# Performance work log

Measured on AMD Instinct MI355X. Metric: run time of the kernel, lower is better.

Reference implementation:

```python
import jax, jax.numpy as jnp
import numpy as np

B_, T_, D_, H_ = 16, 512, 256, 256
SCALE = 0.1


def setup_inputs() -> dict:
    key = jax.random.key(0)
    ks = jax.random.split(key, 4)
    s = 0.05  # xavier-ish init scale
    return {
        "x": jax.random.normal(ks[0], (B_, T_, D_), dtype=jnp.float32),
        "W_w": jax.random.normal(ks[1], (4 * H_, D_), dtype=jnp.float32) * s,
        "W_b": jnp.zeros((4 * H_,), dtype=jnp.float32),
        "U_w": jax.random.normal(ks[2], (4 * H_, H_), dtype=jnp.float32) * s,
        "U_b": jnp.zeros((4 * H_,), dtype=jnp.float32),
        "B_w": jax.random.normal(ks[3], (H_, D_, H_), dtype=jnp.float32) * s,
        "B_b": jnp.zeros((H_,), dtype=jnp.float32),
    }


def reference(x, W_w, W_b, U_w, U_b, B_w, B_b):
    # x: [B,T,D]; W_w: [4H,D]; U_w: [4H,H]; B_w: [H,D,H] (torch Bilinear layout)
    B, T, D = x.shape
    H = U_w.shape[1]
    # Precompute the input projection for all timesteps in one big GEMM
    Wx = jnp.einsum('btd,gd->btg', x, W_w) + W_b  # [B,T,4H]

    def step(carry, inp):
        h, c = carry
        wx_t, x_t = inp  # [B,4H], [B,D]
        gates = wx_t + h @ U_w.T + U_b
        i, f, o, g = jnp.split(gates, 4, axis=-1)
        i = jax.nn.sigmoid(i)
        f = jax.nn.sigmoid(f)
        o = jax.nn.sigmoid(o)
        g = jnp.tanh(g)
        # torch Bilinear: out[b,o] = sum_{d,h} x[b,d] W[o,d,h] h[b,h] + bias
        m = jnp.tanh(jnp.einsum('bd,odh,bh->bo', x_t, B_w, h) + B_b)
        c = f * c + i * g + SCALE * m
        h = o * jnp.tanh(c)
        return (h, c), h

    h0 = jnp.zeros((B, H), dtype=x.dtype)
    c0 = jnp.zeros((B, H), dtype=x.dtype)
    (h, c), outs = jax.lax.scan(
        step, (h0, c0), (jnp.swapaxes(Wx, 0, 1), jnp.swapaxes(x, 0, 1)))
    return jnp.swapaxes(outs, 0, 1), (h, c)  # ([B,T,H], ([B,H],[B,H]))
```

## Files before the change

### kernel.cpp

```cpp
#include <hip/hip_runtime.h>

typedef unsigned short u16;
typedef unsigned int u32;
typedef unsigned long long u64;
typedef short s16x8 __attribute__((ext_vector_type(8)));
typedef float f32x4 __attribute__((ext_vector_type(4)));
typedef __bf16 bf16x2 __attribute__((ext_vector_type(2)));

#define BTH 2097152

__device__ __forceinline__ u16 f2bf(float f) {
  u32 u = __float_as_uint(f);
  u32 r = (u + 0x7FFFu + ((u >> 16) & 1u)) >> 16;
  return (u16)r;
}
__device__ __forceinline__ float bf2f(u16 u) {
  return __uint_as_float(((u32)u) << 16);
}
__device__ __forceinline__ float sigm_(float x) { return 1.f / (1.f + __expf(-x)); }
__device__ __forceinline__ float tanh_(float x) {
  x = fminf(15.f, fmaxf(-15.f, x));
  float e = __expf(2.f * x);
  return (e - 1.f) / (e + 1.f);
}

#if defined(__has_builtin)
#if __has_builtin(__builtin_amdgcn_fdot2_f32_bf16)
#define HAVE_BF16_DOT2 1
#endif
#endif

__device__ __forceinline__ float dotp(u32 a, u32 b, float acc) {
#ifdef HAVE_BF16_DOT2
  return __builtin_amdgcn_fdot2_f32_bf16(__builtin_bit_cast(bf16x2, a),
                                         __builtin_bit_cast(bf16x2, b), acc, false);
#else
  acc += bf2f((u16)(a & 0xFFFFu)) * bf2f((u16)(b & 0xFFFFu));
  acc += bf2f((u16)(a >> 16)) * bf2f((u16)(b >> 16));
  return acc;
#endif
}

__device__ __forceinline__ void async_cp16(const u16* g, u16* l) {
  __builtin_amdgcn_global_load_lds(
      (const __attribute__((address_space(1))) void*)g,
      (__attribute__((address_space(3))) void*)l, 16, 0, 0);
}

__global__ __launch_bounds__(256) void prep_kernel(
    const float* __restrict__ x, const float* __restrict__ Ww,
    const float* __restrict__ Uw, const float* __restrict__ Bw,
    u16* __restrict__ xb, u16* __restrict__ Wbt, u16* __restrict__ Ubt,
    u16* __restrict__ Btt, u64* __restrict__ stz) {
  const int bid = blockIdx.x;
  const int tid = threadIdx.x;
  if (bid < 8192) {
    int e = bid * 256 + tid;
    int d = e & 255;
    int r = e >> 8;
    int bb = r >> 9, t = r & 511;
    xb[(size_t)((t << 4) | bb) * 256 + d] = f2bf(x[e]);
  } else if (bid < 9216) {
    int e = (bid - 8192) * 256 + tid;
    Wbt[e] = f2bf(Ww[e]);
  } else if (bid < 10240) {
    int e = (bid - 9216) * 256 + tid;
    Ubt[e] = f2bf(Uw[e]);
  } else if (bid < 14336) {
    __shared__ float T[64][65];
    int tb = bid - 10240;
    int o = tb >> 4, xi = tb & 15;
    const int d0 = (xi >> 2) * 64;
    const int h0 = (xi & 3) * 64;
    const float* src = Bw + (size_t)o * 65536;
#pragma unroll
    for (int k = 0; k < 16; ++k) {
      int idx = tid + k * 256;
      int rr = idx >> 6, cc = idx & 63;
      T[rr][cc] = src[(size_t)(d0 + rr) * 256 + h0 + cc];
    }
    __syncthreads();
#pragma unroll
    for (int k = 0; k < 16; ++k) {
      int idx = tid + k * 256;
      int rr = idx >> 6, cc = idx & 63;
      Btt[(size_t)(o * 256 + h0 + rr) * 256 + d0 + cc] = f2bf(T[cc][rr]);
    }
  } else {
    for (int i = tid; i < 6144; i += 256) stz[i] = 0ull;
  }
}

__global__ __launch_bounds__(512, 2) void fused_kernel(
    const u16* __restrict__ Ysc, const float* __restrict__ wx,
    const u16* __restrict__ Ubt, const float* __restrict__ Bb,
    float* cbuf, u64* hdata, float* __restrict__ out, int t0, int Tcur,
    const u16* __restrict__ Ag, const u16* __restrict__ Bg,
    u16* __restrict__ Ygm,
    const u16* __restrict__ Wbt, const float* __restrict__ Wb,
    const float* __restrict__ Ub, float* __restrict__ wxout,
    int sblocks, int wxblocks) {
  __shared__ __align__(16) char smem[24576];
  const int tid = threadIdx.x;
  if ((int)blockIdx.x >= sblocks) {
    u16* As = (u16*)smem;
    u16* Bs = (u16*)(smem + 8192);
    const int gi = (int)blockIdx.x - sblocks;
    const bool iswx = gi < wxblocks;
    int mt, n0;
    const u16* Bop;
    if (iswx) {
      mt = gi >> 2;
      n0 = (gi & 3) * 256;
      Bop = Wbt;
    } else {
      int g2 = gi - wxblocks;
      mt = g2 >> 8;
      n0 = (g2 & 255) * 256;
      Bop = Bg;
    }
    const u16* A = Ag + (size_t)mt * 128 * 256;
    const int wave = tid >> 6, lane = tid & 63;
    const int wm = (wave >> 2) * 64, wn = (wave & 3) * 64;
    const int qm = lane & 15, quad = lane >> 4;
    f32x4 acc[4][4] = {};
    const size_t ga = (size_t)(tid >> 2) * 256 + (tid & 3) * 8;
    const int c0 = tid, c1 = tid + 512;
    const size_t gb0 = (size_t)(n0 + (c0 >> 2)) * 256 + (c0 & 3) * 8;
    const size_t gb1 = (size_t)(n0 + (c1 >> 2)) * 256 + (c1 & 3) * 8;
    for (int k0 = 0; k0 < 256; k0 += 32) {
      __syncthreads();
      async_cp16(A + ga + k0, As + tid * 8);
      async_cp16(Bop + gb0 + k0, Bs + c0 * 8);
      async_cp16(Bop + gb1 + k0, Bs + c1 * 8);
      __syncthreads();
      s16x8 af[4], bfr[4];
#pragma unroll
      for (int i = 0; i < 4; ++i)
        af[i] = *(const s16x8*)&As[(wm + i * 16 + qm) * 32 + quad * 8];
#pragma unroll
      for (int j = 0; j < 4; ++j)
        bfr[j] = *(const s16x8*)&Bs[(wn + j * 16 + qm) * 32 + quad * 8];
#pragma unroll
      for (int i = 0; i < 4; ++i)
#pragma unroll
        for (int j = 0; j < 4; ++j)
          acc[i][j] = __builtin_amdgcn_mfma_f32_16x16x32_bf16(af[i], bfr[j], acc[i][j], 0, 0, 0);
    }
    if (iswx) {
#pragma unroll
      for (int i = 0; i < 4; ++i) {
        int rg = mt * 128 + wm + i * 16 + quad * 4;
#pragma unroll
        for (int j = 0; j < 4; ++j) {
          int cg = n0 + wn + j * 16 + qm;
          float bias = Wb[cg] + Ub[cg];
#pragma unroll
          for (int r = 0; r < 4; ++r)
            wxout[(size_t)(rg + r) * 1024 + cg] = acc[i][j][r] + bias;
        }
      }
    } else {
#pragma unroll
      for (int i = 0; i < 4; ++i) {
        int rg = wm + i * 16 + quad * 4;
#pragma unroll
        for (int j = 0; j < 4; ++j) {
          int cg = n0 + wn + j * 16 + qm;
#pragma unroll
          for (int r = 0; r < 4; ++r)
            Ygm[(size_t)(mt * 128 + rg + r) * 65536 + cg] = f2bf(acc[i][j][r]);
        }
      }
    }
    return;
  }
  u32(*lh)[128] = (u32(*)[128])smem;
  int* lflag = (int*)(smem + 1024);
  const int b = blockIdx.x >> 2;
  const int p = blockIdx.x & 3;
  const int oo = tid >> 3;
  const int s = tid & 7;
  const int o = (p << 6) + oo;
  const int wave = tid >> 6;
  const int lane = tid & 63;

  uint4 Ur[4][4];
  const uint4* Ub4 = (const uint4*)Ubt;
#pragma unroll
  for (int g = 0; g < 4; ++g) {
    int row = (g << 8) + o;
#pragma unroll
    for (int j = 0; j < 4; ++j) Ur[g][j] = Ub4[(size_t)row * 32 + s * 4 + j];
  }

  float c = cbuf[(b << 8) + o];
  const float bbias = Bb[o];
  if (tid < 2) lflag[tid] = t0 - 1;

  const int tend = t0 + Tcur;
  const u16* Yp = Ysc + (size_t)b * 65536 + (size_t)o * 256 + s * 32;
  uint4 Yc[4];
  {
    const uint4* y0 = (const uint4*)Yp;
    Yc[0] = y0[0]; Yc[1] = y0[1]; Yc[2] = y0[2]; Yc[3] = y0[3];
  }
  const float* wxp0 = wx + ((size_t)t0 * 16 + b) * 1024 + o;
  float w0 = wxp0[0], w1 = wxp0[256], w2 = wxp0[512], w3 = wxp0[768];
  float hn = 0.f;
  u64* hg = hdata + ((size_t)b << 8);
  __syncthreads();

  for (int t = t0; t < tend; ++t) {
    int dn = (t + 1 < tend) ? (t + 1 - t0) : (t - t0);
    const uint4* ynp = (const uint4*)(Yp + (size_t)dn * 1048576);
    uint4 yn0 = ynp[0], yn1 = ynp[1], yn2 = ynp[2], yn3 = ynp[3];
    int tn = (t + 1 < tend) ? (t + 1) : t;
    const float* nwp = wx + ((size_t)tn * 16 + b) * 1024 + o;
    float nw0 = nwp[0], nw1 = nwp[256], nw2 = nwp[512], nw3 = nwp[768];

    const int par = t & 1;
    if (wave == 0) {
      const u64* hp = hg + (par << 7) + (lane << 1);
      u64 v0, v1;
      for (;;) {
        v0 = __hip_atomic_load(hp, __ATOMIC_RELAXED, __HIP_MEMORY_SCOPE_AGENT);
        v1 = __hip_atomic_load(hp + 1, __ATOMIC_RELAXED, __HIP_MEMORY_SCOPE_AGENT);
        int ok = ((u32)(v0 >> 32) == (u32)t) & ((u32)(v1 >> 32) == (u32)t);
        if (__all(ok)) break;
      }
      lh[par][(lane << 1)] = (u32)v0;
      lh[par][(lane << 1) + 1] = (u32)v1;
      __hip_atomic_store(&lflag[par], t, __ATOMIC_RELEASE, __HIP_MEMORY_SCOPE_WORKGROUP);
    } else {
      while (__hip_atomic_load(&lflag[par], __ATOMIC_ACQUIRE, __HIP_MEMORY_SCOPE_WORKGROUP) < t) {}
    }

    uint4 hq[4];
    {
      const uint4* lp = (const uint4*)&lh[par][s << 4];
      hq[0] = lp[0]; hq[1] = lp[1]; hq[2] = lp[2]; hq[3] = lp[3];
    }

    float a0 = 0.f, a1 = 0.f, a2 = 0.f, a3 = 0.f, am = 0.f;
#pragma unroll
    for (int j = 0; j < 4; ++j) {
      u32 h0 = hq[j].x, h1 = hq[j].y, h2 = hq[j].z, h3 = hq[j].w;
      a0 = dotp(Ur[0][j].x, h0, a0); a0 = dotp(Ur[0][j].y, h1, a0);
      a0 = dotp(Ur[0][j].z, h2, a0); a0 = dotp(Ur[0][j].w, h3, a0);
      a1 = dotp(Ur[1][j].x, h0, a1); a1 = dotp(Ur[1][j].y, h1, a1);
      a1 = dotp(Ur[1][j].z, h2, a1); a1 = dotp(Ur[1][j].w, h3, a1);
      a2 = dotp(Ur[2][j].x, h0, a2); a2 = dotp(Ur[2][j].y, h1, a2);
      a2 = dotp(Ur[2][j].z, h2, a2); a2 = dotp(Ur[2][j].w, h3, a2);
      a3 = dotp(Ur[3][j].x, h0, a3); a3 = dotp(Ur[3][j].y, h1, a3);
      a3 = dotp(Ur[3][j].z, h2, a3); a3 = dotp(Ur[3][j].w, h3, a3);
      am = dotp(Yc[j].x, h0, am);   am = dotp(Yc[j].y, h1, am);
      am = dotp(Yc[j].z, h2, am);   am = dotp(Yc[j].w, h3, am);
    }
#pragma unroll
    for (int mk = 1; mk < 8; mk <<= 1) {
      a0 += __shfl_xor(a0, mk, 8);
      a1 += __shfl_xor(a1, mk, 8);
      a2 += __shfl_xor(a2, mk, 8);
      a3 += __shfl_xor(a3, mk, 8);
      am += __shfl_xor(am, mk, 8);
    }
    float gi = sigm_(a0 + w0);
    float gf = sigm_(a1 + w1);
    float go = sigm_(a2 + w2);
    float gg = tanh_(a3 + w3);
    float mm = tanh_(am + bbias);
    c = gf * c + gi * gg + 0.1f * mm;
    hn = go * tanh_(c);

    float hnext = __shfl_down(hn, 8);
    if (s == 0) {
      if (!(oo & 1)) {
        u32 pk = (u32)f2bf(hn) | ((u32)f2bf(hnext) << 16);
        u64 pk64 = ((u64)(u32)(t + 1) << 32) | (u64)pk;
        __hip_atomic_store(hg + (((size_t)((t + 1) & 1)) << 7) + (p << 5) + (oo >> 1),
                           pk64, __ATOMIC_RELAXED, __HIP_MEMORY_SCOPE_AGENT);
      }
      out[((size_t)b * 512 + t) * 256 + o] = hn;
    }
    Yc[0] = yn0; Yc[1] = yn1; Yc[2] = yn2; Yc[3] = yn3;
    w0 = nw0; w1 = nw1; w2 = nw2; w3 = nw3;
  }
  if (s == 0) {
    cbuf[(b << 8) + o] = c;
    out[(size_t)BTH + (b << 8) + o] = hn;
    out[(size_t)BTH + 4096 + (b << 8) + o] = c;
  }
}

extern "C" void kernel_launch(void* const* d_in, const int* in_sizes, int n_in,
                              void* d_out, int out_size, void* d_ws, size_t ws_size,
                              hipStream_t stream) {
  const float* x  = (const float*)d_in[0];
  const float* Ww = (const float*)d_in[1];
  const float* Wb = (const float*)d_in[2];
  const float* Uw = (const float*)d_in[3];
  const float* Ub = (const float*)d_in[4];
  const float* Bw = (const float*)d_in[5];
  const float* Bb = (const float*)d_in[6];
  float* out = (float*)d_out;

  char* ws = (char*)d_ws;
  const size_t WX_B  = (size_t)512 * 16 * 1024 * 4;
  const size_t XB_B  = (size_t)8192 * 256 * 2;
  const size_t BTT_B = (size_t)65536 * 256 * 2;
  const size_t WBT_B = (size_t)1024 * 256 * 2;
  const size_t UBT_B = (size_t)1024 * 256 * 2;
  const size_t CB_B  = 16384;
  const size_t HD_B  = 32768;
  const size_t ST_B  = CB_B + HD_B;
  const size_t fixedB = WX_B + XB_B + BTT_B + WBT_B + UBT_B + ST_B;
  size_t avail = (ws_size > fixedB) ? (ws_size - fixedB) : 0;
  long Tc = (long)(avail / (2 * 2097152));
  if (Tc > 64) Tc = 64;
  Tc &= ~7L;
  if (Tc < 8) Tc = 8;

  size_t YB   = (size_t)Tc * 2097152;
  u16* Y0     = (u16*)ws;
  u16* Y1     = (u16*)(ws + YB);
  float* wx   = (float*)(ws + 2 * YB);
  u16* xb     = (u16*)(ws + 2 * YB + WX_B);
  u16* Btt    = (u16*)(ws + 2 * YB + WX_B + XB_B);
  u16* Wbt    = (u16*)(ws + 2 * YB + WX_B + XB_B + BTT_B);
  u16* Ubt    = (u16*)(ws + 2 * YB + WX_B + XB_B + BTT_B + WBT_B);
  char* st    = ws + 2 * YB + WX_B + XB_B + BTT_B + WBT_B + UBT_B;
  float* cbuf = (float*)st;
  u64* hdata  = (u64*)(st + CB_B);

  prep_kernel<<<14337, 256, 0, stream>>>(x, Ww, Uw, Bw, xb, Wbt, Ubt, Btt, (u64*)st);

  {
    int Tc0 = (int)Tc;
    int ng0 = (Tc0 * 16 / 128) * 256;
    fused_kernel<<<256 + ng0, 512, 0, stream>>>(
        nullptr, wx, Ubt, Bb, cbuf, hdata, out, 0, 0,
        xb, Btt, Y0, Wbt, Wb, Ub, wx, 0, 256);
  }
  int cidx = 0;
  for (int t0 = 0; t0 < 512; t0 += (int)Tc, ++cidx) {
    int Tcur = (512 - t0 < (int)Tc) ? (512 - t0) : (int)Tc;
    int t0n = t0 + Tcur;
    u16* Ysc = (cidx & 1) ? Y1 : Y0;
    u16* Ygm = (cidx & 1) ? Y0 : Y1;
    int ng = 0;
    const u16* Ag = xb;
    if (t0n < 512) {
      int Tcn = (512 - t0n < (int)Tc) ? (512 - t0n) : (int)Tc;
      ng = (Tcn * 16 / 128) * 256;
      Ag = xb + (size_t)t0n * 4096;
    }
    fused_kernel<<<64 + ng, 512, 0, stream>>>(
        Ysc, wx, Ubt, Bb, cbuf, hdata, out, t0, Tcur,
        Ag, Btt, Ygm, Wbt, Wb, Ub, wx, 64, 0);
  }
}
```

Before: 1.356 ms.

## Process two batch rows per recurrent block to halve recurrent block count

Each recurrent workgroup now handles two independent batch sequences (b and b+8), interleaving their LSTM steps so one sequence's compute can overlap the other's wait for cross-block h exchange. This halves the recurrent blocks from 64 to 32, freeing CUs for the concurrent GEMM blocks. The Y-tile stores from the GEMM path become nontemporal. Per-thread work and register pressure double (two Y caches, two cell states), and the serial per-step latency may grow.

```diff
diff --git a/kernel.cpp b/kernel.cpp
--- a/kernel.cpp
+++ b/kernel.cpp
@@ -45,6 +45,47 @@
   __builtin_amdgcn_global_load_lds(
       (const __attribute__((address_space(1))) void*)g,
       (__attribute__((address_space(3))) void*)l, 16, 0, 0);
+}
+
+__device__ __forceinline__ void lstm_step(
+    const uint4 (&Ur)[4][4], const uint4 (&Yc)[4], const u32* hrow,
+    float w0, float w1, float w2, float w3, float bbias,
+    float& c, float& hn) {
+  uint4 hq[4];
+  {
+    const uint4* lp = (const uint4*)hrow;
+    hq[0] = lp[0]; hq[1] = lp[1]; hq[2] = lp[2]; hq[3] = lp[3];
+  }
+  float a0 = 0.f, a1 = 0.f, a2 = 0.f, a3 = 0.f, am = 0.f;
+#pragma unroll
+  for (int j = 0; j < 4; ++j) {
+    u32 h0 = hq[j].x, h1 = hq[j].y, h2 = hq[j].z, h3 = hq[j].w;
+    a0 = dotp(Ur[0][j].x, h0, a0); a0 = dotp(Ur[0][j].y, h1, a0);
+    a0 = dotp(Ur[0][j].z, h2, a0); a0 = dotp(Ur[0][j].w, h3, a0);
+    a1 = dotp(Ur[1][j].x, h0, a1); a1 = dotp(Ur[1][j].y, h1, a1);
+    a1 = dotp(Ur[1][j].z, h2, a1); a1 = dotp(Ur[1][j].w, h3, a1);
+    a2 = dotp(Ur[2][j].x, h0, a2); a2 = dotp(Ur[2][j].y, h1, a2);
+    a2 = dotp(Ur[2][j].z, h2, a2); a2 = dotp(Ur[2][j].w, h3, a2);
+    a3 = dotp(Ur[3][j].x, h0, a3); a3 = dotp(Ur[3][j].y, h1, a3);
+    a3 = dotp(Ur[3][j].z, h2, a3); a3 = dotp(Ur[3][j].w, h3, a3);
+    am = dotp(Yc[j].x, h0, am);   am = dotp(Yc[j].y, h1, am);
+    am = dotp(Yc[j].z, h2, am);   am = dotp(Yc[j].w, h3, am);
+  }
+#pragma unroll
+  for (int mk = 1; mk < 8; mk <<= 1) {
+    a0 += __shfl_xor(a0, mk, 8);
+    a1 += __shfl_xor(a1, mk, 8);
+    a2 += __shfl_xor(a2, mk, 8);
+    a3 += __shfl_xor(a3, mk, 8);
+    am += __shfl_xor(am, mk, 8);
+  }
+  float gi = sigm_(a0 + w0);
+  float gf = sigm_(a1 + w1);
+  float go = sigm_(a2 + w2);
+  float gg = tanh_(a3 + w3);
+  float mm = tanh_(am + bbias);
+  c = gf * c + gi * gg + 0.1f * mm;
+  hn = go * tanh_(c);
 }
 
 __global__ __launch_bounds__(256) void prep_kernel(
@@ -169,15 +210,17 @@
           int cg = n0 + wn + j * 16 + qm;
 #pragma unroll
           for (int r = 0; r < 4; ++r)
-            Ygm[(size_t)(mt * 128 + rg + r) * 65536 + cg] = f2bf(acc[i][j][r]);
+            __builtin_nontemporal_store(
+                f2bf(acc[i][j][r]),
+                &Ygm[(size_t)(mt * 128 + rg + r) * 65536 + cg]);
         }
       }
     }
     return;
   }
-  u32(*lh)[128] = (u32(*)[128])smem;
-  int* lflag = (int*)(smem + 1024);
-  const int b = blockIdx.x >> 2;
+  u32(*lh)[2][128] = (u32(*)[2][128])smem;
+  int* lflag = (int*)(smem + 4096);
+  const int bh = blockIdx.x >> 2;
   const int p = blockIdx.x & 3;
   const int oo = tid >> 3;
   const int s = tid & 7;
@@ -194,34 +237,34 @@
     for (int j = 0; j < 4; ++j) Ur[g][j] = Ub4[(size_t)row * 32 + s * 4 + j];
   }
 
-  float c = cbuf[(b << 8) + o];
   const float bbias = Bb[o];
-  if (tid < 2) lflag[tid] = t0 - 1;
+  float cA = cbuf[(bh << 8) + o];
+  float cB = cbuf[((bh + 8) << 8) + o];
+  if (tid < 4) lflag[tid] = t0 - 1;
 
   const int tend = t0 + Tcur;
-  const u16* Yp = Ysc + (size_t)b * 65536 + (size_t)o * 256 + s * 32;
-  uint4 Yc[4];
+  const u16* YpA = Ysc + (size_t)bh * 65536 + (size_t)o * 256 + s * 32;
+  const u16* YpB = YpA + (size_t)8 * 65536;
+  uint4 YcA[4], YcB[4];
   {
-    const uint4* y0 = (const uint4*)Yp;
-    Yc[0] = y0[0]; Yc[1] = y0[1]; Yc[2] = y0[2]; Yc[3] = y0[3];
-  }
-  const float* wxp0 = wx + ((size_t)t0 * 16 + b) * 1024 + o;
-  float w0 = wxp0[0], w1 = wxp0[256], w2 = wxp0[512], w3 = wxp0[768];
-  float hn = 0.f;
-  u64* hg = hdata + ((size_t)b << 8);
+    const uint4* ya = (const uint4*)YpA;
+    YcA[0] = ya[0]; YcA[1] = ya[1]; YcA[2] = ya[2]; YcA[3] = ya[3];
+    const uint4* yb = (const uint4*)YpB;
+    YcB[0] = yb[0]; YcB[1] = yb[1]; YcB[2] = yb[2]; YcB[3] = yb[3];
+  }
+  const float* wxpA0 = wx + ((size_t)t0 * 16 + bh) * 1024 + o;
+  float wA0 = wxpA0[0], wA1 = wxpA0[256], wA2 = wxpA0[512], wA3 = wxpA0[768];
+  const float* wxpB0 = wxpA0 + 8 * 1024;
+  float wB0 = wxpB0[0], wB1 = wxpB0[256], wB2 = wxpB0[512], wB3 = wxpB0[768];
+  float hnA = 0.f, hnB = 0.f;
+  u64* hgA = hdata + ((size_t)bh << 8);
+  u64* hgB = hdata + ((size_t)(bh + 8) << 8);
   __syncthreads();
 
   for (int t = t0; t < tend; ++t) {
-    int dn = (t + 1 < tend) ? (t + 1 - t0) : (t - t0);
-    const uint4* ynp = (const uint4*)(Yp + (size_t)dn * 1048576);
-    uint4 yn0 = ynp[0], yn1 = ynp[1], yn2 = ynp[2], yn3 = ynp[3];
-    int tn = (t + 1 < tend) ? (t + 1) : t;
-    const float* nwp = wx + ((size_t)tn * 16 + b) * 1024 + o;
-    float nw0 = nwp[0], nw1 = nwp[256], nw2 = nwp[512], nw3 = nwp[768];
-
     const int par = t & 1;
     if (wave == 0) {
-      const u64* hp = hg + (par << 7) + (lane << 1);
+      const u64* hp = hgA + (par << 7) + (lane << 1);
       u64 v0, v1;
       for (;;) {
         v0 = __hip_atomic_load(hp, __ATOMIC_RELAXED, __HIP_MEMORY_SCOPE_AGENT);
@@ -229,67 +272,74 @@
         int ok = ((u32)(v0 >> 32) == (u32)t) & ((u32)(v1 >> 32) == (u32)t);
         if (__all(ok)) break;
       }
-      lh[par][(lane << 1)] = (u32)v0;
-      lh[par][(lane << 1) + 1] = (u32)v1;
+      lh[0][par][(lane << 1)] = (u32)v0;
+      lh[0][par][(lane << 1) + 1] = (u32)v1;
       __hip_atomic_store(&lflag[par], t, __ATOMIC_RELEASE, __HIP_MEMORY_SCOPE_WORKGROUP);
-    } else {
-      while (__hip_atomic_load(&lflag[par], __ATOMIC_ACQUIRE, __HIP_MEMORY_SCOPE_WORKGROUP) < t) {}
-    }
-
-    uint4 hq[4];
+    } else if (wave == 1) {
+      const u64* hp = hgB + (par << 7) + (lane << 1);
+      u64 v0, v1;
+      for (;;) {
+        v0 = __hip_atomic_load(hp, __ATOMIC_RELAXED, __HIP_MEMORY_SCOPE_AGENT);
+        v1 = __hip_atomic_load(hp + 1, __ATOMIC_RELAXED, __HIP_MEMORY_SCOPE_AGENT);
+        int ok = ((u32)(v0 >> 32) == (u32)t) & ((u32)(v1 >> 32) == (u32)t);
+        if (__all(ok)) break;
+      }
+      lh[1][par][(lane << 1)] = (u32)v0;
+      lh[1][par][(lane << 1) + 1] = (u32)v1;
+      __hip_atomic_store(&lflag[2 + par], t, __ATOMIC_RELEASE, __HIP_MEMORY_SCOPE_WORKGROUP);
+    }
+    int dn = (t + 1 < tend) ? (t + 1 - t0) : (t - t0);
+    int tn = (t + 1 < tend) ? (t + 1) : t;
+
+    while (__hip_atomic_load(&lflag[par], __ATOMIC_ACQUIRE, __HIP_MEMORY_SCOPE_WORKGROUP) < t) {}
+    lstm_step(Ur, YcA, &lh[0][par][s << 4], wA0, wA1, wA2, wA3, bbias, cA, hnA);
     {
-      const uint4* lp = (const uint4*)&lh[par][s << 4];
-      hq[0] = lp[0]; hq[1] = lp[1]; hq[2] = lp[2]; hq[3] = lp[3];
-    }
-
-    float a0 = 0.f, a1 = 0.f, a2 = 0.f, a3 = 0.f, am = 0.f;
-#pragma unroll
-    for (int j = 0; j < 4; ++j) {
-      u32 h0 = hq[j].x, h1 = hq[j].y, h2 = hq[j].z, h3 = hq[j].w;
-      a0 = dotp(Ur[0][j].x, h0, a0); a0 = dotp(Ur[0][j].y, h1, a0);
-      a0 = dotp(Ur[0][j].z, h2, a0); a0 = dotp(Ur[0][j].w, h3, a0);
-      a1 = dotp(Ur[1][j].x, h0, a1); a1 = dotp(Ur[1][j].y, h1, a1);
-      a1 = dotp(Ur[1][j].z, h2, a1); a1 = dotp(Ur[1][j].w, h3, a1);
-      a2 = dotp(Ur[2][j].x, h0, a2); a2 = dotp(Ur[2][j].y, h1, a2);
-      a2 = dotp(Ur[2][j].z, h2, a2); a2 = dotp(Ur[2][j].w, h3, a2);
-      a3 = dotp(Ur[3][j].x, h0, a3); a3 = dotp(Ur[3][j].y, h1, a3);
-      a3 = dotp(Ur[3][j].z, h2, a3); a3 = dotp(Ur[3][j].w, h3, a3);
-      am = dotp(Yc[j].x, h0, am);   am = dotp(Yc[j].y, h1, am);
-      am = dotp(Yc[j].z, h2, am);   am = dotp(Yc[j].w, h3, am);
-    }
-#pragma unroll
-    for (int mk = 1; mk < 8; mk <<= 1) {
-      a0 += __shfl_xor(a0, mk, 8);
-      a1 += __shfl_xor(a1, mk, 8);
-      a2 += __shfl_xor(a2, mk, 8);
-      a3 += __shfl_xor(a3, mk, 8);
-      am += __shfl_xor(am, mk, 8);
-    }
-    float gi = sigm_(a0 + w0);
-    float gf = sigm_(a1 + w1);
-    float go = sigm_(a2 + w2);
-    float gg = tanh_(a3 + w3);
-    float mm = tanh_(am + bbias);
-    c = gf * c + gi * gg + 0.1f * mm;
-    hn = go * tanh_(c);
-
-    float hnext = __shfl_down(hn, 8);
-    if (s == 0) {
-      if (!(oo & 1)) {
-        u32 pk = (u32)f2bf(hn) | ((u32)f2bf(hnext) << 16);
-        u64 pk64 = ((u64)(u32)(t + 1) << 32) | (u64)pk;
-        __hip_atomic_store(hg + (((size_t)((t + 1) & 1)) << 7) + (p << 5) + (oo >> 1),
-                           pk64, __ATOMIC_RELAXED, __HIP_MEMORY_SCOPE_AGENT);
-      }
-      out[((size_t)b * 512 + t) * 256 + o] = hn;
-    }
-    Yc[0] = yn0; Yc[1] = yn1; Yc[2] = yn2; Yc[3] = yn3;
-    w0 = nw0; w1 = nw1; w2 = nw2; w3 = nw3;
+      float hnext = __shfl_down(hnA, 8);
+      if (s == 0) {
+        if (!(oo & 1)) {
+          u32 pk = (u32)f2bf(hnA) | ((u32)f2bf(hnext) << 16);
+          u64 pk64 = ((u64)(u32)(t + 1) << 32) | (u64)pk;
+          __hip_atomic_store(hgA + (((size_t)((t + 1) & 1)) << 7) + (p << 5) + (oo >> 1),
+                             pk64, __ATOMIC_RELAXED, __HIP_MEMORY_SCOPE_AGENT);
+        }
+        out[((size_t)bh * 512 + t) * 256 + o] = hnA;
+      }
+    }
+    {
+      const uint4* ynp = (const uint4*)(YpA + (size_t)dn * 1048576);
+      YcA[0] = ynp[0]; YcA[1] = ynp[1]; YcA[2] = ynp[2]; YcA[3] = ynp[3];
+      const float* nwp = wx + ((size_t)tn * 16 + bh) * 1024 + o;
+      wA0 = nwp[0]; wA1 = nwp[256]; wA2 = nwp[512]; wA3 = nwp[768];
+    }
+
+    while (__hip_atomic_load(&lflag[2 + par], __ATOMIC_ACQUIRE, __HIP_MEMORY_SCOPE_WORKGROUP) < t) {}
+    lstm_step(Ur, YcB, &lh[1][par][s << 4], wB0, wB1, wB2, wB3, bbias, cB, hnB);
+    {
+      float hnext = __shfl_down(hnB, 8);
+      if (s == 0) {
+        if (!(oo & 1)) {
+          u32 pk = (u32)f2bf(hnB) | ((u32)f2bf(hnext) << 16);
+          u64 pk64 = ((u64)(u32)(t + 1) << 32) | (u64)pk;
+          __hip_atomic_store(hgB + (((size_t)((t + 1) & 1)) << 7) + (p << 5) + (oo >> 1),
+                             pk64, __ATOMIC_RELAXED, __HIP_MEMORY_SCOPE_AGENT);
+        }
+        out[((size_t)(bh + 8) * 512 + t) * 256 + o] = hnB;
+      }
+    }
+    {
+      const uint4* ynp = (const uint4*)(YpB + (size_t)dn * 1048576);
+      YcB[0] = ynp[0]; YcB[1] = ynp[1]; YcB[2] = ynp[2]; YcB[3] = ynp[3];
+      const float* nwp = wx + ((size_t)tn * 16 + bh + 8) * 1024 + o;
+      wB0 = nwp[0]; wB1 = nwp[256]; wB2 = nwp[512]; wB3 = nwp[768];
+    }
   }
   if (s == 0) {
-    cbuf[(b << 8) + o] = c;
-    out[(size_t)BTH + (b << 8) + o] = hn;
-    out[(size_t)BTH + 4096 + (b << 8) + o] = c;
+    cbuf[(bh << 8) + o] = cA;
+    cbuf[((bh + 8) << 8) + o] = cB;
+    out[(size_t)BTH + (bh << 8) + o] = hnA;
+    out[(size_t)BTH + 4096 + (bh << 8) + o] = cA;
+    out[(size_t)BTH + ((bh + 8) << 8) + o] = hnB;
+    out[(size_t)BTH + 4096 + ((bh + 8) << 8) + o] = cB;
   }
 }
 
@@ -355,8 +405,8 @@
       ng = (Tcn * 16 / 128) * 256;
       Ag = xb + (size_t)t0n * 4096;
     }
-    fused_kernel<<<64 + ng, 512, 0, stream>>>(
+    fused_kernel<<<32 + ng, 512, 0, stream>>>(
         Ysc, wx, Ubt, Bb, cbuf, hdata, out, t0, Tcur,
-        Ag, Btt, Ygm, Wbt, Wb, Ub, wx, 64, 0);
-  }
-}
+        Ag, Btt, Ygm, Wbt, Wb, Ub, wx, 32, 0);
+  }
+}
```

Result: slower. 1.997 ms (+47.3%).

## Add L2-scoped fast polling path for hidden-state exchange with fallback

Applied to the files above, without the earlier changes.

Adds a second hidden-state buffer written with a plain volatile store and polled with sc0 global loads (L2-level coherence) instead of agent-scope atomics, falling back to the original atomic buffer after 200 failed spins. Block-to-(batch, slice) mapping is also changed so the four blocks sharing a batch are spread across block indices, likely to place cooperating blocks on different XCDs or the same L2. The aim is lower cross-block synchronization latency on each recurrent timestep, at the cost of extra stores and reliance on cache coherence assumptions that may not hold across XCDs, in which case the fallback adds 200 wasted polls once.

```diff
diff --git a/kernel.cpp b/kernel.cpp
--- a/kernel.cpp
+++ b/kernel.cpp
@@ -45,6 +45,16 @@
   __builtin_amdgcn_global_load_lds(
       (const __attribute__((address_space(1))) void*)g,
       (__attribute__((address_space(3))) void*)l, 16, 0, 0);
+}
+
+__device__ __forceinline__ void l2_load2(const u64* p0, u64& v0, u64& v1) {
+  asm volatile(
+      "global_load_dwordx2 %0, %2, off sc0\n\t"
+      "global_load_dwordx2 %1, %3, off sc0\n\t"
+      "s_waitcnt vmcnt(0)"
+      : "=&v"(v0), "=&v"(v1)
+      : "v"(p0), "v"(p0 + 1)
+      : "memory");
 }
 
 __global__ __launch_bounds__(256) void prep_kernel(
@@ -87,14 +97,15 @@
       Btt[(size_t)(o * 256 + h0 + rr) * 256 + d0 + cc] = f2bf(T[cc][rr]);
     }
   } else {
-    for (int i = tid; i < 6144; i += 256) stz[i] = 0ull;
+    for (int i = tid; i < 10240; i += 256) stz[i] = 0ull;
   }
 }
 
 __global__ __launch_bounds__(512, 2) void fused_kernel(
     const u16* __restrict__ Ysc, const float* __restrict__ wx,
     const u16* __restrict__ Ubt, const float* __restrict__ Bb,
-    float* cbuf, u64* hdata, float* __restrict__ out, int t0, int Tcur,
+    float* cbuf, u64* hdata, u64* hfast, float* __restrict__ out,
+    int t0, int Tcur,
     const u16* __restrict__ Ag, const u16* __restrict__ Bg,
     u16* __restrict__ Ygm,
     const u16* __restrict__ Wbt, const float* __restrict__ Wb,
@@ -177,8 +188,8 @@
   }
   u32(*lh)[128] = (u32(*)[128])smem;
   int* lflag = (int*)(smem + 1024);
-  const int b = blockIdx.x >> 2;
-  const int p = blockIdx.x & 3;
+  const int b = blockIdx.x & 15;
+  const int p = blockIdx.x >> 4;
   const int oo = tid >> 3;
   const int s = tid & 7;
   const int o = (p << 6) + oo;
@@ -209,6 +220,8 @@
   float w0 = wxp0[0], w1 = wxp0[256], w2 = wxp0[512], w3 = wxp0[768];
   float hn = 0.f;
   u64* hg = hdata + ((size_t)b << 8);
+  u64* hf = hfast + ((size_t)b << 8);
+  bool fastok = true;
   __syncthreads();
 
   for (int t = t0; t < tend; ++t) {
@@ -221,13 +234,26 @@
 
     const int par = t & 1;
     if (wave == 0) {
-      const u64* hp = hg + (par << 7) + (lane << 1);
-      u64 v0, v1;
-      for (;;) {
-        v0 = __hip_atomic_load(hp, __ATOMIC_RELAXED, __HIP_MEMORY_SCOPE_AGENT);
-        v1 = __hip_atomic_load(hp + 1, __ATOMIC_RELAXED, __HIP_MEMORY_SCOPE_AGENT);
-        int ok = ((u32)(v0 >> 32) == (u32)t) & ((u32)(v1 >> 32) == (u32)t);
-        if (__all(ok)) break;
+      u64 v0 = 0, v1 = 0;
+      bool got = false;
+      if (fastok && t != t0) {
+        const u64* fp = hf + (par << 7) + (lane << 1);
+        int it = 0;
+        for (;;) {
+          l2_load2(fp, v0, v1);
+          int ok = ((u32)(v0 >> 32) == (u32)t) & ((u32)(v1 >> 32) == (u32)t);
+          if (__all(ok)) { got = true; break; }
+          if (++it == 200) { fastok = false; break; }
+        }
+      }
+      if (!got) {
+        const u64* hp = hg + (par << 7) + (lane << 1);
+        for (;;) {
+          v0 = __hip_atomic_load(hp, __ATOMIC_RELAXED, __HIP_MEMORY_SCOPE_AGENT);
+          v1 = __hip_atomic_load(hp + 1, __ATOMIC_RELAXED, __HIP_MEMORY_SCOPE_AGENT);
+          int ok = ((u32)(v0 >> 32) == (u32)t) & ((u32)(v1 >> 32) == (u32)t);
+          if (__all(ok)) break;
+        }
       }
       lh[par][(lane << 1)] = (u32)v0;
       lh[par][(lane << 1) + 1] = (u32)v1;
@@ -278,8 +304,10 @@
       if (!(oo & 1)) {
         u32 pk = (u32)f2bf(hn) | ((u32)f2bf(hnext) << 16);
         u64 pk64 = ((u64)(u32)(t + 1) << 32) | (u64)pk;
-        __hip_atomic_store(hg + (((size_t)((t + 1) & 1)) << 7) + (p << 5) + (oo >> 1),
-                           pk64, __ATOMIC_RELAXED, __HIP_MEMORY_SCOPE_AGENT);
+        size_t hidx = (((size_t)((t + 1) & 1)) << 7) + (p << 5) + (oo >> 1);
+        *(volatile u64*)(hf + hidx) = pk64;
+        __hip_atomic_store(hg + hidx, pk64, __ATOMIC_RELAXED,
+                           __HIP_MEMORY_SCOPE_AGENT);
       }
       out[((size_t)b * 512 + t) * 256 + o] = hn;
     }
@@ -313,7 +341,8 @@
   const size_t UBT_B = (size_t)1024 * 256 * 2;
   const size_t CB_B  = 16384;
   const size_t HD_B  = 32768;
-  const size_t ST_B  = CB_B + HD_B;
+  const size_t HF_B  = 32768;
+  const size_t ST_B  = CB_B + HD_B + HF_B;
   const size_t fixedB = WX_B + XB_B + BTT_B + WBT_B + UBT_B + ST_B;
   size_t avail = (ws_size > fixedB) ? (ws_size - fixedB) : 0;
   long Tc = (long)(avail / (2 * 2097152));
@@ -332,6 +361,7 @@
   char* st    = ws + 2 * YB + WX_B + XB_B + BTT_B + WBT_B + UBT_B;
   float* cbuf = (float*)st;
   u64* hdata  = (u64*)(st + CB_B);
+  u64* hfast  = (u64*)(st + CB_B + HD_B);
 
   prep_kernel<<<14337, 256, 0, stream>>>(x, Ww, Uw, Bw, xb, Wbt, Ubt, Btt, (u64*)st);
 
@@ -339,7 +369,7 @@
     int Tc0 = (int)Tc;
     int ng0 = (Tc0 * 16 / 128) * 256;
     fused_kernel<<<256 + ng0, 512, 0, stream>>>(
-        nullptr, wx, Ubt, Bb, cbuf, hdata, out, 0, 0,
+        nullptr, wx, Ubt, Bb, cbuf, hdata, hfast, out, 0, 0,
         xb, Btt, Y0, Wbt, Wb, Ub, wx, 0, 256);
   }
   int cidx = 0;
@@ -356,7 +386,7 @@
       Ag = xb + (size_t)t0n * 4096;
     }
     fused_kernel<<<64 + ng, 512, 0, stream>>>(
-        Ysc, wx, Ubt, Bb, cbuf, hdata, out, t0, Tcur,
+        Ysc, wx, Ubt, Bb, cbuf, hdata, hfast, out, t0, Tcur,
         Ag, Btt, Ygm, Wbt, Wb, Ub, wx, 64, 0);
   }
 }
```

Result: slower. 1.755 ms (+29.4%).
